# Performance work log

Measured on AMD Instinct MI355X. Metric: run time of the kernel, lower is better.

Reference implementation:

```python
import jax, jax.numpy as jnp
import numpy as np

EMBED = 64
HEADS = 8
DHEAD = EMBED // HEADS  # 8
LAYERS = 4
VOCAB = 32000
SEQ = 1024
BATCH = 8
EPS = 1e-5


def setup_inputs() -> dict:
    key = jax.random.key(0)
    ks = jax.random.split(key, 24)
    s = 0.02
    inp = {
        "x": jax.random.randint(ks[0], (BATCH, SEQ), 0, VOCAB),
        "targets": jax.random.randint(ks[1], (BATCH, SEQ), 0, VOCAB),
        "tok_emb": jax.random.normal(ks[2], (VOCAB, EMBED)) * s,
        "pos_emb": jax.random.normal(ks[3], (SEQ, EMBED)) * s,
        # per-layer, per-head q/k/v projections (stored as (in,out) so y = x @ W + b)
        "Wq": jax.random.normal(ks[4], (LAYERS, HEADS, EMBED, DHEAD)) * s,
        "bq": jax.random.normal(ks[5], (LAYERS, HEADS, DHEAD)) * s,
        "Wk": jax.random.normal(ks[6], (LAYERS, HEADS, EMBED, DHEAD)) * s,
        "bk": jax.random.normal(ks[7], (LAYERS, HEADS, DHEAD)) * s,
        "Wv": jax.random.normal(ks[8], (LAYERS, HEADS, EMBED, DHEAD)) * s,
        "bv": jax.random.normal(ks[9], (LAYERS, HEADS, DHEAD)) * s,
        "ln1_g": jnp.ones((LAYERS, EMBED)) + jax.random.normal(ks[10], (LAYERS, EMBED)) * s,
        "ln1_b": jax.random.normal(ks[11], (LAYERS, EMBED)) * s,
        "ln2_g": jnp.ones((LAYERS, EMBED)) + jax.random.normal(ks[12], (LAYERS, EMBED)) * s,
        "ln2_b": jax.random.normal(ks[13], (LAYERS, EMBED)) * s,
        "W1": jax.random.normal(ks[14], (LAYERS, EMBED, 4 * EMBED)) * s,
        "b1": jax.random.normal(ks[15], (LAYERS, 4 * EMBED)) * s,
        "W2": jax.random.normal(ks[16], (LAYERS, 4 * EMBED, EMBED)) * s,
        "b2": jax.random.normal(ks[17], (LAYERS, EMBED)) * s,
        "Wout": jax.random.normal(ks[18], (EMBED, VOCAB)) * s,
        "bout": jax.random.normal(ks[19], (VOCAB,)) * s,
    }
    return inp


def _layernorm(x, g, b):
    mu = jnp.mean(x, axis=-1, keepdims=True)
    var = jnp.var(x, axis=-1, keepdims=True)
    return (x - mu) / jnp.sqrt(var + EPS) * g + b


def _mha(h, Wq, bq, Wk, bk, Wv, bv):
    B, T, C = h.shape
    q = jnp.einsum('btc,hcd->bhtd', h, Wq) + bq[:, None, :]
    k = jnp.einsum('btc,hcd->bhtd', h, Wk) + bk[:, None, :]
    v = jnp.einsum('btc,hcd->bhtd', h, Wv) + bv[:, None, :]
    # FAITHFUL to source: key output is .view(B, C, T) -- a raw reshape, not transpose
    kr = k.reshape(B, HEADS, DHEAD, T)
    w = jnp.einsum('bhtd,bhds->bhts', q, kr)  # [B,H,T,T]
    w = jnp.tril(w)
    w = jnp.where(w == 0, -jnp.inf, w)
    w = jax.nn.softmax(w / np.sqrt(DHEAD), axis=-1)
    o = jnp.einsum('bhts,bhsd->bhtd', w, v)
    return o.transpose(0, 2, 1, 3).reshape(B, T, HEADS * DHEAD)


def _forward(x, targets, tok_emb, pos_emb, Wq, bq, Wk, bk, Wv, bv,
             ln1_g, ln1_b, ln2_g, ln2_b, W1, b1, W2, b2, Wout, bout):
    B, T = x.shape
    h = tok_emb[x] + pos_emb[:T]
    for l in range(LAYERS):
        h = h + _layernorm(_mha(h, Wq[l], bq[l], Wk[l], bk[l], Wv[l], bv[l]), ln1_g[l], ln1_b[l])
        z = _layernorm(h, ln2_g[l], ln2_b[l])
        h = h + jax.nn.relu(z @ W1[l] + b1[l]) @ W2[l] + b2[l]
    logits = h @ Wout + bout  # [B,T,V]
    lp = jax.nn.log_softmax(logits.reshape(B * T, -1), axis=-1)
    nll = -jnp.take_along_axis(lp, targets.reshape(B * T, 1), axis=1)
    loss = jnp.mean(nll)
    return logits, loss


def reference(x, targets, tok_emb, pos_emb, Wq, bq, Wk, bk, Wv, bv,
              ln1_g, ln1_b, ln2_g, ln2_b, W1, b1, W2, b2, Wout, bout):
    return _forward(x, targets, tok_emb, pos_emb, Wq, bq, Wk, bk, Wv, bv,
                    ln1_g, ln1_b, ln2_g, ln2_b, W1, b1, W2, b2, Wout, bout)
```

## Files before the change

kernel.cpp:

```cpp
#include <hip/hip_runtime.h>
#include <hip/hip_bf16.h>
#include <math.h>

#define BB 8
#define TT 1024
#define CC 64
#define HH 8
#define DH 8
#define NLAY 4
#define VV 32000
#define FF 256
#define NR (BB*TT)
#define NLOGIT 262144000
#define NCB 125

typedef unsigned short u16;
typedef unsigned int u32;
typedef __attribute__((ext_vector_type(8))) short short8v;
typedef __attribute__((ext_vector_type(4))) float f32x4;

__device__ __forceinline__ float b2f(u16 u){
  union { float f; u32 i; } c; c.i = ((u32)u) << 16; return c.f;
}
__device__ __forceinline__ u16 f2b(float f){
  union { float f; u32 i; } c; c.f = f;
  u32 x = c.i;
  return (u16)((x + 0x7FFF + ((x >> 16) & 1)) >> 16);
}
__device__ __forceinline__ u32 pack2(float lo, float hi){
  return (u32)f2b(lo) | ((u32)f2b(hi) << 16);
}
__device__ __forceinline__ int probe_bf16(const void* ln1g){
  const u16* lp = (const u16*)ln1g;
  unsigned long long m = __ballot((lp[threadIdx.x & 63] >> 8) == 0x3F);
  return (__popcll(m) > 48) ? 1 : 0;
}

struct ConvArgs {
  const void* src[18];
  float* dst[18];
  int n[18];
  int blkoff[19];
};
__global__ void k_convert(ConvArgs a, const void* ln1g){
  int isb = probe_bf16(ln1g);
  int bid = blockIdx.x;
  int t = 0;
  while (bid >= a.blkoff[t + 1]) t++;
  int base = (bid - a.blkoff[t]) * 1024 + threadIdx.x;
  const u16* s16 = (const u16*)a.src[t];
  const float* s32 = (const float*)a.src[t];
  float* d = a.dst[t];
  int n = a.n[t];
  #pragma unroll
  for (int e = 0; e < 4; e++){
    int i = base + e * 256;
    if (i < n) d[i] = isb ? b2f(s16[i]) : s32[i];
  }
}

__global__ void __launch_bounds__(256) k_trans(const void* __restrict__ wsrc, const void* __restrict__ ln1g,
                                               u16* __restrict__ wt){
  __shared__ float ws_[64][65];
  int tid = threadIdx.x;
  int isb = probe_bf16(ln1g);
  int v0 = blockIdx.x * 64;
  const u16* s16 = (const u16*)wsrc;
  const float* s32 = (const float*)wsrc;
  int vl = tid & 63;
  #pragma unroll
  for (int kk = 0; kk < 16; kk++){
    int k = kk * 4 + (tid >> 6);
    size_t idx = (size_t)k * VV + v0 + vl;
    ws_[vl][k] = isb ? b2f(s16[idx]) : s32[idx];
  }
  __syncthreads();
  #pragma unroll
  for (int pass = 0; pass < 16; pass++){
    int v2 = pass * 4 + (tid >> 6);
    int k = tid & 63;
    wt[(size_t)(v0 + v2) * 64 + k] = f2b(ws_[v2][k]);
  }
}

__global__ void k_embed(const int* __restrict__ x, const float* __restrict__ tok,
                        const float* __restrict__ pos, float* __restrict__ h){
  int i = blockIdx.x * 256 + threadIdx.x;
  int r = i >> 6, c = i & 63;
  int t = r & (TT - 1);
  h[i] = tok[x[r] * 64 + c] + pos[t * 64 + c];
}

__global__ void k_qkv(const float* __restrict__ h,
                      const float* __restrict__ wq, const float* __restrict__ bq,
                      const float* __restrict__ wk, const float* __restrict__ bk,
                      const float* __restrict__ wv, const float* __restrict__ bv,
                      u16* __restrict__ q16, u16* __restrict__ kp16, u16* __restrict__ vt16){
  __shared__ float hs[4][64];
  int tid = threadIdx.x;
  int row0 = blockIdx.x * 4;
  hs[tid >> 6][tid & 63] = h[row0 * 64 + tid];
  __syncthreads();
  int rr = tid >> 6, o = tid & 63;
  int head = o >> 3, d = o & 7;
  int row = row0 + rr;
  int b = row >> 10, t = row & (TT - 1);
  float aq = bq[head * 8 + d], ak = bk[head * 8 + d], av = bv[head * 8 + d];
  #pragma unroll
  for (int c = 0; c < 64; c++){
    float hv = hs[rr][c];
    aq += hv * wq[(head * 64 + c) * 8 + d];
    ak += hv * wk[(head * 64 + c) * 8 + d];
    av += hv * wv[(head * 64 + c) * 8 + d];
  }
  int bh = b * HH + head;
  q16[((size_t)bh * TT + t) * 8 + d] = f2b(aq * 0.35355339059327378f);
  int i = t * 8 + d;
  kp16[((size_t)bh * TT + (i & 1023)) * 8 + (i >> 10)] = f2b(ak);
  vt16[((size_t)bh * 8 + d) * TT + t] = f2b(av);
}

__global__ void __launch_bounds__(512) k_attn2(const u16* __restrict__ q16, const u16* __restrict__ kp16,
                                               const u16* __restrict__ vt16, const float* __restrict__ g,
                                               const float* __restrict__ be, float* __restrict__ h){
  __shared__ float ot[16][64];
  int tid = threadIdx.x;
  int w = tid >> 6;
  int lane = tid & 63;
  int lr = lane & 15, lg = lane >> 4;
  int b = blockIdx.y;
  int bh = b * HH + w;
  int tb = blockIdx.x * 16;
  int t_g = tb + lr;

  short8v qf = {0,0,0,0,0,0,0,0};
  if (lg == 0) qf = *(const short8v*)(q16 + ((size_t)bh * TT + tb + lr) * 8);

  float m = -1e30f, l = 0.f;
  f32x4 o = {0.f, 0.f, 0.f, 0.f};
  int nchunk = (tb >> 5) + 1;

  for (int c = 0; c < nchunk; c++){
    int s0 = c * 32;
    bool skipB = (s0 + 16 > tb + 15);
    short8v kA = {0,0,0,0,0,0,0,0}, kB = {0,0,0,0,0,0,0,0};
    if (lg == 0){
      kA = *(const short8v*)(kp16 + ((size_t)bh * TT + s0 + lr) * 8);
      if (!skipB) kB = *(const short8v*)(kp16 + ((size_t)bh * TT + s0 + 16 + lr) * 8);
    }
    f32x4 sA = __builtin_amdgcn_mfma_f32_16x16x32_bf16(kA, qf, (f32x4){0.f,0.f,0.f,0.f}, 0, 0, 0);
    f32x4 sB;
    if (!skipB)
      sB = __builtin_amdgcn_mfma_f32_16x16x32_bf16(kB, qf, (f32x4){0.f,0.f,0.f,0.f}, 0, 0, 0);
    else
      sB = (f32x4){-1e30f, -1e30f, -1e30f, -1e30f};

    if (s0 + 15 > tb){
      #pragma unroll
      for (int r = 0; r < 4; r++) if (s0 + lg * 4 + r > t_g) sA[r] = -1e30f;
    }
    if (!skipB && s0 + 31 > tb){
      #pragma unroll
      for (int r = 0; r < 4; r++) if (s0 + 16 + lg * 4 + r > t_g) sB[r] = -1e30f;
    }

    float tm = fmaxf(fmaxf(fmaxf(sA[0], sA[1]), fmaxf(sA[2], sA[3])),
                     fmaxf(fmaxf(sB[0], sB[1]), fmaxf(sB[2], sB[3])));
    tm = fmaxf(tm, __shfl_xor(tm, 16, 64));
    tm = fmaxf(tm, __shfl_xor(tm, 32, 64));
    float mn = fmaxf(m, tm);
    float fac = __expf(m - mn);
    l *= fac;
    {
      float f0 = __shfl(fac, lg * 4 + 0, 64);
      float f1 = __shfl(fac, lg * 4 + 1, 64);
      float f2 = __shfl(fac, lg * 4 + 2, 64);
      float f3 = __shfl(fac, lg * 4 + 3, 64);
      o[0] *= f0; o[1] *= f1; o[2] *= f2; o[3] *= f3;
    }
    f32x4 pA, pB;
    #pragma unroll
    for (int r = 0; r < 4; r++){ pA[r] = __expf(sA[r] - mn); pB[r] = __expf(sB[r] - mn); }
    float ls = pA[0] + pA[1] + pA[2] + pA[3] + pB[0] + pB[1] + pB[2] + pB[3];
    ls += __shfl_xor(ls, 16, 64);
    ls += __shfl_xor(ls, 32, 64);
    l += ls;
    m = mn;

    u32 a0 = pack2(pA[0], pA[1]), a1 = pack2(pA[2], pA[3]);
    u32 b0 = pack2(pB[0], pB[1]), b1 = pack2(pB[2], pB[3]);
    int src0 = ((2 * lg) & 3) * 16 + lr;
    int src1 = src0 + 16;
    u32 A0 = __shfl((int)a0, src0, 64), A1 = __shfl((int)a1, src0, 64);
    u32 A2 = __shfl((int)a0, src1, 64), A3 = __shfl((int)a1, src1, 64);
    u32 B0 = __shfl((int)b0, src0, 64), B1 = __shfl((int)b1, src0, 64);
    u32 B2 = __shfl((int)b0, src1, 64), B3 = __shfl((int)b1, src1, 64);
    union { u32 u[4]; short8v v; } pu;
    if (lg < 2){ pu.u[0] = A0; pu.u[1] = A1; pu.u[2] = A2; pu.u[3] = A3; }
    else       { pu.u[0] = B0; pu.u[1] = B1; pu.u[2] = B2; pu.u[3] = B3; }

    short8v vf = {0,0,0,0,0,0,0,0};
    if (lr < 8) vf = *(const short8v*)(vt16 + ((size_t)bh * 8 + lr) * TT + s0 + lg * 8);

    o = __builtin_amdgcn_mfma_f32_16x16x32_bf16(pu.v, vf, o, 0, 0, 0);
  }

  float linv = 1.f / l;
  float i0 = __shfl(linv, lg * 4 + 0, 64);
  float i1 = __shfl(linv, lg * 4 + 1, 64);
  float i2 = __shfl(linv, lg * 4 + 2, 64);
  float i3 = __shfl(linv, lg * 4 + 3, 64);
  if (lr < 8){
    ot[lg * 4 + 0][w * 8 + lr] = o[0] * i0;
    ot[lg * 4 + 1][w * 8 + lr] = o[1] * i1;
    ot[lg * 4 + 2][w * 8 + lr] = o[2] * i2;
    ot[lg * 4 + 3][w * 8 + lr] = o[3] * i3;
  }
  __syncthreads();

  #pragma unroll
  for (int pass = 0; pass < 2; pass++){
    int rl = (tid >> 6) + pass * 8;
    float x = ot[rl][lane];
    float s = x, sq = x * x;
    for (int msk = 32; msk; msk >>= 1){
      s += __shfl_xor(s, msk, 64);
      sq += __shfl_xor(sq, msk, 64);
    }
    float mu = s * (1.f / 64);
    float var = sq * (1.f / 64) - mu * mu;
    float rstd = rsqrtf(fmaxf(var, 0.f) + 1e-5f);
    h[((size_t)b * TT + tb + rl) * 64 + lane] += (x - mu) * rstd * g[lane] + be[lane];
  }
}

__global__ void k_ffn(float* __restrict__ h, const float* __restrict__ g, const float* __restrict__ bb,
                      const float* __restrict__ w1, const float* __restrict__ b1,
                      const float* __restrict__ w2, const float* __restrict__ b2,
                      u16* __restrict__ hbo, int last){
  __shared__ float z[8][64];
  __shared__ float a[8][256];
  int tid = threadIdx.x;
  int row0 = blockIdx.x * 8;
  {
    int rr = tid >> 5, cp = tid & 31;
    int c0 = cp * 2;
    const float* hp = h + (row0 + rr) * 64;
    float x0 = hp[c0], x1 = hp[c0 + 1];
    float s = x0 + x1, sq = x0 * x0 + x1 * x1;
    for (int msk = 16; msk; msk >>= 1){
      s += __shfl_xor(s, msk, 64);
      sq += __shfl_xor(sq, msk, 64);
    }
    float mu = s * (1.f / 64);
    float var = sq * (1.f / 64) - mu * mu;
    float rstd = rsqrtf(fmaxf(var, 0.f) + 1e-5f);
    z[rr][c0]     = (x0 - mu) * rstd * g[c0] + bb[c0];
    z[rr][c0 + 1] = (x1 - mu) * rstd * g[c0 + 1] + bb[c0 + 1];
  }
  __syncthreads();
  {
    int j = tid;
    float acc[8];
    float bj = b1[j];
    #pragma unroll
    for (int r = 0; r < 8; r++) acc[r] = bj;
    for (int c = 0; c < 64; c++){
      float w = w1[c * 256 + j];
      #pragma unroll
      for (int r = 0; r < 8; r++) acc[r] += z[r][c] * w;
    }
    #pragma unroll
    for (int r = 0; r < 8; r++) a[r][j] = fmaxf(acc[r], 0.f);
  }
  __syncthreads();
  #pragma unroll
  for (int half = 0; half < 2; half++){
    int oi = tid + half * 256;
    int r = oi >> 6, c = oi & 63;
    float acc = b2[c];
    for (int k = 0; k < 256; k++) acc += a[r][k] * w2[k * 64 + c];
    int gi = (row0 + r) * 64 + c;
    float nh = h[gi] + acc;
    h[gi] = nh;
    if (last) hbo[gi] = f2b(nh);
  }
}

__global__ void __launch_bounds__(256) k_logits(const u16* __restrict__ hb, const u16* __restrict__ wt,
                                                const float* __restrict__ bout, float* __restrict__ logits,
                                                float2* __restrict__ part){
  int tid = threadIdx.x;
  int wave = tid >> 6, lane = tid & 63;
  int lr = lane & 15, lg = lane >> 4;
  int row0 = blockIdx.x * 64;
  int cb = blockIdx.y;
  int colw = cb * 256 + wave * 64;

  short8v hf[4][2];
  #pragma unroll
  for (int ri = 0; ri < 4; ri++)
    #pragma unroll
    for (int kk = 0; kk < 2; kk++)
      hf[ri][kk] = *(const short8v*)(hb + (row0 + ri * 16 + lr) * 64 + kk * 32 + lg * 8);

  short8v wfr[4][2];
  #pragma unroll
  for (int vi = 0; vi < 4; vi++)
    #pragma unroll
    for (int kk = 0; kk < 2; kk++)
      wfr[vi][kk] = *(const short8v*)(wt + (size_t)(colw + vi * 16 + lr) * 64 + kk * 32 + lg * 8);

  f32x4 acc[4][4];
  #pragma unroll
  for (int ri = 0; ri < 4; ri++)
    #pragma unroll
    for (int vi = 0; vi < 4; vi++)
      acc[ri][vi] = (f32x4){0.f, 0.f, 0.f, 0.f};

  #pragma unroll
  for (int ri = 0; ri < 4; ri++){
    #pragma unroll
    for (int vi = 0; vi < 4; vi++){
      acc[ri][vi] = __builtin_amdgcn_mfma_f32_16x16x32_bf16(wfr[vi][0], hf[ri][0], acc[ri][vi], 0, 0, 0);
      acc[ri][vi] = __builtin_amdgcn_mfma_f32_16x16x32_bf16(wfr[vi][1], hf[ri][1], acc[ri][vi], 0, 0, 0);
    }
  }

  f32x4 bo[4];
  #pragma unroll
  for (int vi = 0; vi < 4; vi++)
    bo[vi] = *(const f32x4*)(bout + colw + vi * 16 + lg * 4);

  __shared__ float2 wml[4][64];
  #pragma unroll
  for (int ri = 0; ri < 4; ri++){
    f32x4 vals[4];
    #pragma unroll
    for (int vi = 0; vi < 4; vi++){
      vals[vi] = acc[ri][vi] + bo[vi];
      __builtin_nontemporal_store(vals[vi],
        (f32x4*)(logits + (size_t)(row0 + ri * 16 + lr) * VV + colw + vi * 16 + lg * 4));
    }
    float mx = -1e30f;
    #pragma unroll
    for (int vi = 0; vi < 4; vi++)
      #pragma unroll
      for (int r = 0; r < 4; r++) mx = fmaxf(mx, vals[vi][r]);
    mx = fmaxf(mx, __shfl_xor(mx, 16, 64));
    mx = fmaxf(mx, __shfl_xor(mx, 32, 64));
    float sume = 0.f;
    #pragma unroll
    for (int vi = 0; vi < 4; vi++)
      #pragma unroll
      for (int r = 0; r < 4; r++) sume += __expf(vals[vi][r] - mx);
    sume += __shfl_xor(sume, 16, 64);
    sume += __shfl_xor(sume, 32, 64);
    if (lg == 0) wml[wave][ri * 16 + lr] = make_float2(mx, sume);
  }
  __syncthreads();
  if (tid < 64){
    float M = -1e30f;
    #pragma unroll
    for (int w = 0; w < 4; w++) M = fmaxf(M, wml[w][tid].x);
    float L = 0.f;
    #pragma unroll
    for (int w = 0; w < 4; w++){
      float2 p = wml[w][tid];
      L += p.y * __expf(p.x - M);
    }
    part[(size_t)cb * NR + row0 + tid] = make_float2(M, L);
  }
}

__global__ void k_loss(const float2* __restrict__ part, const float* __restrict__ logits,
                       const int* __restrict__ tgt, float* __restrict__ lpart){
  int row = blockIdx.x * 64 + (threadIdx.x & 63);
  float M = -1e30f;
  for (int j = 0; j < NCB; j++) M = fmaxf(M, part[(size_t)j * NR + row].x);
  float L = 0.f;
  for (int j = 0; j < NCB; j++){
    float2 p = part[(size_t)j * NR + row];
    L += p.y * __expf(p.x - M);
  }
  float lse = M + __logf(L);
  float tl = logits[(size_t)row * VV + tgt[row]];
  float nll = lse - tl;
  for (int msk = 32; msk; msk >>= 1) nll += __shfl_xor(nll, msk, 64);
  if ((threadIdx.x & 63) == 0) lpart[blockIdx.x] = nll;
}
__global__ void k_loss2(const float* __restrict__ lpart, float* __restrict__ out){
  int lane = threadIdx.x & 63;
  float s = lpart[lane] + lpart[lane + 64];
  for (int msk = 32; msk; msk >>= 1) s += __shfl_xor(s, msk, 64);
  if (lane == 0) out[NLOGIT] = s * (1.f / NR);
}

extern "C" void kernel_launch(void* const* d_in, const int* in_sizes, int n_in,
                              void* d_out, int out_size, void* d_ws, size_t ws_size,
                              hipStream_t stream){
  (void)in_sizes; (void)n_in; (void)out_size; (void)ws_size;
  const int* x = (const int*)d_in[0];
  const int* targets = (const int*)d_in[1];
  float* out = (float*)d_out;

  static const int WN[18] = {2048000, 65536, 16384, 256, 16384, 256, 16384, 256,
                             256, 256, 256, 256, 65536, 1024, 65536, 256, 0, 32000};
  char* ws = (char*)d_ws;
  size_t off = 0;
  auto alloc = [&](size_t bytes) -> void* {
    void* p = ws + off;
    off += (bytes + 255) & ~(size_t)255;
    return p;
  };
  float* wf[18];
  for (int i = 0; i < 18; i++) wf[i] = (float*)alloc((size_t)(WN[i] ? WN[i] : 1) * 4);
  float* h     = (float*)alloc((size_t)NR * 64 * 4);
  u16* q16     = (u16*)alloc((size_t)NR * 64 * 2);
  u16* kp16    = (u16*)alloc((size_t)NR * 64 * 2);
  u16* vt16    = (u16*)alloc((size_t)NR * 64 * 2);
  u16* hb      = (u16*)alloc((size_t)NR * 64 * 2);
  u16* wt16    = (u16*)alloc((size_t)2048000 * 2);
  float2* part = (float2*)alloc((size_t)NCB * NR * 8);
  float* lpart = (float*)alloc(128 * 4);

  ConvArgs ca;
  int blk = 0;
  for (int i = 0; i < 18; i++){
    ca.src[i] = d_in[2 + i];
    ca.dst[i] = wf[i];
    ca.n[i] = WN[i];
    ca.blkoff[i] = blk;
    blk += (WN[i] + 1023) / 1024;
  }
  ca.blkoff[18] = blk;
  hipLaunchKernelGGL(k_convert, dim3(blk), dim3(256), 0, stream, ca, d_in[10]);
  hipLaunchKernelGGL(k_trans, dim3(500), dim3(256), 0, stream, d_in[18], d_in[10], wt16);
  hipLaunchKernelGGL(k_embed, dim3(2048), dim3(256), 0, stream, x, wf[0], wf[1], h);

  for (int l = 0; l < NLAY; l++){
    hipLaunchKernelGGL(k_qkv, dim3(2048), dim3(256), 0, stream, h,
                       wf[2] + l * 4096, wf[3] + l * 64,
                       wf[4] + l * 4096, wf[5] + l * 64,
                       wf[6] + l * 4096, wf[7] + l * 64,
                       q16, kp16, vt16);
    hipLaunchKernelGGL(k_attn2, dim3(64, 8), dim3(512), 0, stream, q16, kp16, vt16,
                       wf[8] + l * 64, wf[9] + l * 64, h);
    hipLaunchKernelGGL(k_ffn, dim3(1024), dim3(256), 0, stream, h,
                       wf[10] + l * 64, wf[11] + l * 64,
                       wf[12] + l * 16384, wf[13] + l * 256,
                       wf[14] + l * 16384, wf[15] + l * 64,
                       hb, (l == NLAY - 1) ? 1 : 0);
  }

  hipLaunchKernelGGL(k_logits, dim3(128, NCB), dim3(256), 0, stream, hb, wt16, wf[17], out, part);
  hipLaunchKernelGGL(k_loss, dim3(128), dim3(64), 0, stream, part, out, targets, lpart);
  hipLaunchKernelGGL(k_loss2, dim3(1), dim3(64), 0, stream, lpart, out);
}
```

Before: 735.2 us.

## Fuse FFN into attention kernel, merge convert/transpose, embed from raw inputs

The FFN (layernorm2, W1+ReLU, W2, residual) now runs inside the attention kernel, so each block keeps its 16 rows in shared memory instead of a separate kernel re-reading h. The weight-convert and Wout-transpose kernels are merged into one launch. The embedding kernel reads tok/pos embeddings directly from the inputs, which drops converting the large token table. The trade-off is fewer FFN blocks (512 vs 1024) with more shared memory each, which may lower occupancy for the attention part.

```diff
diff --git a/kernel.cpp b/kernel.cpp
--- a/kernel.cpp
+++ b/kernel.cpp
@@ -18,6 +18,7 @@
 typedef unsigned int u32;
 typedef __attribute__((ext_vector_type(8))) short short8v;
 typedef __attribute__((ext_vector_type(4))) float f32x4;
+typedef __attribute__((ext_vector_type(2))) float f32x2;
 
 __device__ __forceinline__ float b2f(u16 u){
   union { float f; u32 i; } c; c.i = ((u32)u) << 16; return c.f;
@@ -42,53 +43,59 @@
   int n[18];
   int blkoff[19];
 };
-__global__ void k_convert(ConvArgs a, const void* ln1g){
+__global__ void __launch_bounds__(256) k_convtrans(ConvArgs a, const void* __restrict__ wsrc,
+                                                   const void* __restrict__ ln1g, u16* __restrict__ wt){
+  __shared__ float ws_[64][65];
   int isb = probe_bf16(ln1g);
-  int bid = blockIdx.x;
-  int t = 0;
-  while (bid >= a.blkoff[t + 1]) t++;
-  int base = (bid - a.blkoff[t]) * 1024 + threadIdx.x;
-  const u16* s16 = (const u16*)a.src[t];
-  const float* s32 = (const float*)a.src[t];
-  float* d = a.dst[t];
-  int n = a.n[t];
-  #pragma unroll
-  for (int e = 0; e < 4; e++){
-    int i = base + e * 256;
-    if (i < n) d[i] = isb ? b2f(s16[i]) : s32[i];
-  }
-}
-
-__global__ void __launch_bounds__(256) k_trans(const void* __restrict__ wsrc, const void* __restrict__ ln1g,
-                                               u16* __restrict__ wt){
-  __shared__ float ws_[64][65];
+  int nconv = a.blkoff[18];
   int tid = threadIdx.x;
+  if ((int)blockIdx.x < nconv){
+    int bid = blockIdx.x;
+    int t = 0;
+    while (bid >= a.blkoff[t + 1]) t++;
+    int base = (bid - a.blkoff[t]) * 1024 + tid;
+    const u16* s16 = (const u16*)a.src[t];
+    const float* s32 = (const float*)a.src[t];
+    float* d = a.dst[t];
+    int n = a.n[t];
+    #pragma unroll
+    for (int e = 0; e < 4; e++){
+      int i = base + e * 256;
+      if (i < n) d[i] = isb ? b2f(s16[i]) : s32[i];
+    }
+  } else {
+    int v0 = (blockIdx.x - nconv) * 64;
+    const u16* s16 = (const u16*)wsrc;
+    const float* s32 = (const float*)wsrc;
+    int vl = tid & 63;
+    #pragma unroll
+    for (int kk = 0; kk < 16; kk++){
+      int k = kk * 4 + (tid >> 6);
+      size_t idx = (size_t)k * VV + v0 + vl;
+      ws_[vl][k] = isb ? b2f(s16[idx]) : s32[idx];
+    }
+    __syncthreads();
+    #pragma unroll
+    for (int pass = 0; pass < 16; pass++){
+      int v2 = pass * 4 + (tid >> 6);
+      int k = tid & 63;
+      wt[(size_t)(v0 + v2) * 64 + k] = f2b(ws_[v2][k]);
+    }
+  }
+}
+
+__global__ void k_embed(const int* __restrict__ x, const void* __restrict__ tokr,
+                        const void* __restrict__ posr, const void* __restrict__ ln1g,
+                        float* __restrict__ h){
   int isb = probe_bf16(ln1g);
-  int v0 = blockIdx.x * 64;
-  const u16* s16 = (const u16*)wsrc;
-  const float* s32 = (const float*)wsrc;
-  int vl = tid & 63;
-  #pragma unroll
-  for (int kk = 0; kk < 16; kk++){
-    int k = kk * 4 + (tid >> 6);
-    size_t idx = (size_t)k * VV + v0 + vl;
-    ws_[vl][k] = isb ? b2f(s16[idx]) : s32[idx];
-  }
-  __syncthreads();
-  #pragma unroll
-  for (int pass = 0; pass < 16; pass++){
-    int v2 = pass * 4 + (tid >> 6);
-    int k = tid & 63;
-    wt[(size_t)(v0 + v2) * 64 + k] = f2b(ws_[v2][k]);
-  }
-}
-
-__global__ void k_embed(const int* __restrict__ x, const float* __restrict__ tok,
-                        const float* __restrict__ pos, float* __restrict__ h){
   int i = blockIdx.x * 256 + threadIdx.x;
   int r = i >> 6, c = i & 63;
   int t = r & (TT - 1);
-  h[i] = tok[x[r] * 64 + c] + pos[t * 64 + c];
+  size_t ti = (size_t)x[r] * 64 + c;
+  size_t pi = (size_t)t * 64 + c;
+  float tv = isb ? b2f(((const u16*)tokr)[ti]) : ((const float*)tokr)[ti];
+  float pv = isb ? b2f(((const u16*)posr)[pi]) : ((const float*)posr)[pi];
+  h[i] = tv + pv;
 }
 
 __global__ void k_qkv(const float* __restrict__ h,
@@ -120,10 +127,16 @@
   vt16[((size_t)bh * 8 + d) * TT + t] = f2b(av);
 }
 
-__global__ void __launch_bounds__(512) k_attn2(const u16* __restrict__ q16, const u16* __restrict__ kp16,
-                                               const u16* __restrict__ vt16, const float* __restrict__ g,
-                                               const float* __restrict__ be, float* __restrict__ h){
+__global__ void __launch_bounds__(512) k_layer(const u16* __restrict__ q16, const u16* __restrict__ kp16,
+                                               const u16* __restrict__ vt16,
+                                               const float* __restrict__ g1, const float* __restrict__ be1,
+                                               const float* __restrict__ g2, const float* __restrict__ be2,
+                                               const float* __restrict__ w1, const float* __restrict__ b1,
+                                               const float* __restrict__ w2, const float* __restrict__ b2,
+                                               float* __restrict__ h, u16* __restrict__ hbo, int last){
   __shared__ float ot[16][64];
+  __shared__ float z[16][64];
+  __shared__ float a[16][256];
   int tid = threadIdx.x;
   int w = tid >> 6;
   int lane = tid & 63;
@@ -188,13 +201,13 @@
     m = mn;
 
     u32 a0 = pack2(pA[0], pA[1]), a1 = pack2(pA[2], pA[3]);
-    u32 b0 = pack2(pB[0], pB[1]), b1 = pack2(pB[2], pB[3]);
+    u32 b0 = pack2(pB[0], pB[1]), b1v = pack2(pB[2], pB[3]);
     int src0 = ((2 * lg) & 3) * 16 + lr;
     int src1 = src0 + 16;
     u32 A0 = __shfl((int)a0, src0, 64), A1 = __shfl((int)a1, src0, 64);
     u32 A2 = __shfl((int)a0, src1, 64), A3 = __shfl((int)a1, src1, 64);
-    u32 B0 = __shfl((int)b0, src0, 64), B1 = __shfl((int)b1, src0, 64);
-    u32 B2 = __shfl((int)b0, src1, 64), B3 = __shfl((int)b1, src1, 64);
+    u32 B0 = __shfl((int)b0, src0, 64), B1 = __shfl((int)b1v, src0, 64);
+    u32 B2 = __shfl((int)b0, src1, 64), B3 = __shfl((int)b1v, src1, 64);
     union { u32 u[4]; short8v v; } pu;
     if (lg < 2){ pu.u[0] = A0; pu.u[1] = A1; pu.u[2] = A2; pu.u[3] = A3; }
     else       { pu.u[0] = B0; pu.u[1] = B1; pu.u[2] = B2; pu.u[3] = B3; }
@@ -220,7 +233,7 @@
 
   #pragma unroll
   for (int pass = 0; pass < 2; pass++){
-    int rl = (tid >> 6) + pass * 8;
+    int rl = w + pass * 8;
     float x = ot[rl][lane];
     float s = x, sq = x * x;
     for (int msk = 32; msk; msk >>= 1){
@@ -230,60 +243,59 @@
     float mu = s * (1.f / 64);
     float var = sq * (1.f / 64) - mu * mu;
     float rstd = rsqrtf(fmaxf(var, 0.f) + 1e-5f);
-    h[((size_t)b * TT + tb + rl) * 64 + lane] += (x - mu) * rstd * g[lane] + be[lane];
-  }
-}
-
-__global__ void k_ffn(float* __restrict__ h, const float* __restrict__ g, const float* __restrict__ bb,
-                      const float* __restrict__ w1, const float* __restrict__ b1,
-                      const float* __restrict__ w2, const float* __restrict__ b2,
-                      u16* __restrict__ hbo, int last){
-  __shared__ float z[8][64];
-  __shared__ float a[8][256];
-  int tid = threadIdx.x;
-  int row0 = blockIdx.x * 8;
+    float hres = h[((size_t)b * TT + tb + rl) * 64 + lane] + (x - mu) * rstd * g1[lane] + be1[lane];
+    ot[rl][lane] = hres;
+    float s2 = hres, sq2 = hres * hres;
+    for (int msk = 32; msk; msk >>= 1){
+      s2 += __shfl_xor(s2, msk, 64);
+      sq2 += __shfl_xor(sq2, msk, 64);
+    }
+    float mu2 = s2 * (1.f / 64);
+    float var2 = sq2 * (1.f / 64) - mu2 * mu2;
+    float rstd2 = rsqrtf(fmaxf(var2, 0.f) + 1e-5f);
+    z[rl][lane] = (hres - mu2) * rstd2 * g2[lane] + be2[lane];
+  }
+  __syncthreads();
+
   {
-    int rr = tid >> 5, cp = tid & 31;
-    int c0 = cp * 2;
-    const float* hp = h + (row0 + rr) * 64;
-    float x0 = hp[c0], x1 = hp[c0 + 1];
-    float s = x0 + x1, sq = x0 * x0 + x1 * x1;
-    for (int msk = 16; msk; msk >>= 1){
-      s += __shfl_xor(s, msk, 64);
-      sq += __shfl_xor(sq, msk, 64);
-    }
-    float mu = s * (1.f / 64);
-    float var = sq * (1.f / 64) - mu * mu;
-    float rstd = rsqrtf(fmaxf(var, 0.f) + 1e-5f);
-    z[rr][c0]     = (x0 - mu) * rstd * g[c0] + bb[c0];
-    z[rr][c0 + 1] = (x1 - mu) * rstd * g[c0 + 1] + bb[c0 + 1];
+    int row = tid >> 5;
+    int j0 = (tid & 31) * 8;
+    float acc[8];
+    #pragma unroll
+    for (int i = 0; i < 8; i++) acc[i] = b1[j0 + i];
+    for (int c = 0; c < 64; c++){
+      float zv = z[row][c];
+      const f32x4* wv = (const f32x4*)(w1 + c * 256 + j0);
+      f32x4 w0 = wv[0], w1v = wv[1];
+      #pragma unroll
+      for (int i = 0; i < 4; i++) acc[i] += zv * w0[i];
+      #pragma unroll
+      for (int i = 0; i < 4; i++) acc[4 + i] += zv * w1v[i];
+    }
+    #pragma unroll
+    for (int i = 0; i < 8; i++) a[row][j0 + i] = fmaxf(acc[i], 0.f);
   }
   __syncthreads();
+
   {
-    int j = tid;
-    float acc[8];
-    float bj = b1[j];
-    #pragma unroll
-    for (int r = 0; r < 8; r++) acc[r] = bj;
-    for (int c = 0; c < 64; c++){
-      float w = w1[c * 256 + j];
-      #pragma unroll
-      for (int r = 0; r < 8; r++) acc[r] += z[r][c] * w;
-    }
-    #pragma unroll
-    for (int r = 0; r < 8; r++) a[r][j] = fmaxf(acc[r], 0.f);
-  }
-  __syncthreads();
-  #pragma unroll
-  for (int half = 0; half < 2; half++){
-    int oi = tid + half * 256;
-    int r = oi >> 6, c = oi & 63;
-    float acc = b2[c];
-    for (int k = 0; k < 256; k++) acc += a[r][k] * w2[k * 64 + c];
-    int gi = (row0 + r) * 64 + c;
-    float nh = h[gi] + acc;
-    h[gi] = nh;
-    if (last) hbo[gi] = f2b(nh);
+    int row = tid >> 5;
+    int c0 = (tid & 31) * 2;
+    float acc0 = b2[c0], acc1 = b2[c0 + 1];
+    for (int k = 0; k < 256; k++){
+      float av = a[row][k];
+      f32x2 wv = *(const f32x2*)(w2 + k * 64 + c0);
+      acc0 += av * wv[0];
+      acc1 += av * wv[1];
+    }
+    size_t gi = ((size_t)b * TT + tb + row) * 64 + c0;
+    float h0 = ot[row][c0] + acc0;
+    float h1 = ot[row][c0 + 1] + acc1;
+    h[gi] = h0;
+    h[gi + 1] = h1;
+    if (last){
+      hbo[gi] = f2b(h0);
+      hbo[gi + 1] = f2b(h1);
+    }
   }
 }
 
@@ -404,7 +416,7 @@
   const int* targets = (const int*)d_in[1];
   float* out = (float*)d_out;
 
-  static const int WN[18] = {2048000, 65536, 16384, 256, 16384, 256, 16384, 256,
+  static const int WN[18] = {0, 0, 16384, 256, 16384, 256, 16384, 256,
                              256, 256, 256, 256, 65536, 1024, 65536, 256, 0, 32000};
   char* ws = (char*)d_ws;
   size_t off = 0;
@@ -434,9 +446,8 @@
     blk += (WN[i] + 1023) / 1024;
   }
   ca.blkoff[18] = blk;
-  hipLaunchKernelGGL(k_convert, dim3(blk), dim3(256), 0, stream, ca, d_in[10]);
-  hipLaunchKernelGGL(k_trans, dim3(500), dim3(256), 0, stream, d_in[18], d_in[10], wt16);
-  hipLaunchKernelGGL(k_embed, dim3(2048), dim3(256), 0, stream, x, wf[0], wf[1], h);
+  hipLaunchKernelGGL(k_convtrans, dim3(blk + 500), dim3(256), 0, stream, ca, d_in[18], d_in[10], wt16);
+  hipLaunchKernelGGL(k_embed, dim3(2048), dim3(256), 0, stream, x, d_in[2], d_in[3], d_in[10], h);
 
   for (int l = 0; l < NLAY; l++){
     hipLaunchKernelGGL(k_qkv, dim3(2048), dim3(256), 0, stream, h,
@@ -444,13 +455,12 @@
                        wf[4] + l * 4096, wf[5] + l * 64,
                        wf[6] + l * 4096, wf[7] + l * 64,
                        q16, kp16, vt16);
-    hipLaunchKernelGGL(k_attn2, dim3(64, 8), dim3(512), 0, stream, q16, kp16, vt16,
-                       wf[8] + l * 64, wf[9] + l * 64, h);
-    hipLaunchKernelGGL(k_ffn, dim3(1024), dim3(256), 0, stream, h,
+    hipLaunchKernelGGL(k_layer, dim3(64, 8), dim3(512), 0, stream, q16, kp16, vt16,
+                       wf[8] + l * 64, wf[9] + l * 64,
                        wf[10] + l * 64, wf[11] + l * 64,
                        wf[12] + l * 16384, wf[13] + l * 256,
                        wf[14] + l * 16384, wf[15] + l * 64,
-                       hb, (l == NLAY - 1) ? 1 : 0);
+                       h, hb, (l == NLAY - 1) ? 1 : 0);
   }
 
   hipLaunchKernelGGL(k_logits, dim3(128, NCB), dim3(256), 0, stream, hb, wt16, wf[17], out, part);
```

Measured after the change: 788.4 us. 7.2% more time.
